# Kernel optimization log

Measured on AMD Instinct MI355X. Metric: run time of the kernel, lower is better.

The kernel has to match this reference:

```python
import jax, jax.numpy as jnp
import numpy as np

PAD = 2  # matches init_kwargs padding

# HEALPix face layout (DLWP-HEALPix / earth2grid convention):
#   faces 0-3 : northern polar cap
#   faces 4-7 : equatorial belt
#   faces 8-11: southern polar cap
# Padding each face gathers edge strips from topological neighbor faces;
# polar-cap neighbors require 90/180-degree rotations, and the two degenerate
# equatorial corners (touching a pole vertex, 3 faces meet) are filled with
# edge continuations + an averaged corner pixel.

def _rot(x, k):
    return jnp.rot90(x, k, axes=(-2, -1))

def _corner_tl(t, l, p):
    # degenerate top-left corner of an equatorial face (pole vertex)
    shp = t.shape[:-2] + (p, p)
    c = jnp.zeros(shp, t.dtype)
    c = c.at[..., :, -1].set(t[..., -p:, 0])          # continue top neighbor's left edge
    c = c.at[..., -1, :].set(l[..., 0, -p:])          # continue left neighbor's top edge
    c = c.at[..., -1, -1].set(0.5 * t[..., -1, 0] + 0.5 * l[..., 0, -1])
    return c

def _corner_br(b, r, p):
    # degenerate bottom-right corner of an equatorial face (pole vertex)
    shp = b.shape[:-2] + (p, p)
    c = jnp.zeros(shp, b.dtype)
    c = c.at[..., :, 0].set(b[..., :p, -1])
    c = c.at[..., 0, :].set(r[..., -1, :p])
    c = c.at[..., 0, 0].set(0.5 * b[..., 0, -1] + 0.5 * r[..., -1, 0])
    return c

def _assemble(tl, t, tr, l, c, r, bl, b, br):
    top = jnp.concatenate([tl, t, tr], axis=-1)
    mid = jnp.concatenate([l, c, r], axis=-1)
    bot = jnp.concatenate([bl, b, br], axis=-1)
    return jnp.concatenate([top, mid, bot], axis=-2)

def _pn(c, t, tl, l, bl, b, br, r, tr, p):
    # northern polar face: top/left neighbors are rotated polar faces
    return _assemble(
        _rot(tl, 2)[..., -p:, -p:], _rot(t, 1)[..., -p:, :], _rot(tr, 1)[..., -p:, :p],
        _rot(l, -1)[..., :, -p:],   c,                       r[..., :, :p],
        bl[..., :p, -p:],           b[..., :p, :],           br[..., :p, :p])

def _pe(c, t, tl, l, bl, b, br, r, tr, p):
    # equatorial face: no rotations; tl/br are precomputed degenerate corners
    return _assemble(
        tl,               t[..., -p:, :], tr[..., -p:, :p],
        l[..., :, -p:],   c,              r[..., :, :p],
        bl[..., :p, -p:], b[..., :p, :],  br)

def _ps(c, t, tl, l, bl, b, br, r, tr, p):
    # southern polar face: mirror image of the northern case
    return _assemble(
        tl[..., -p:, :p], t[..., -p:, :],        tr[..., -p:, -p:],
        l[..., :, -p:],   c,                     _rot(r, -1)[..., :, :p],
        _rot(bl, 1)[..., :p, -p:], _rot(b, 1)[..., :p, :], _rot(br, 2)[..., :p, :p])

def healpix_pad(x, p):
    # x: (B, 12, C, H, W) -> (B, 12, C, H+2p, W+2p)
    f = [x[:, i] for i in range(12)]
    out = []
    for i in range(4):  # northern cap faces 0..3
        out.append(_pn(f[i], t=f[(i + 1) % 4], tl=f[(i + 2) % 4], l=f[(i - 1) % 4],
                       bl=f[(i - 1) % 4], b=f[4 + i], br=f[8 + i],
                       r=f[4 + (i + 1) % 4], tr=f[(i + 1) % 4], p=p))
    for i in range(4):  # equatorial faces 4..7
        out.append(_pe(f[4 + i], t=f[i], tl=_corner_tl(f[i], f[(i - 1) % 4], p),
                       l=f[(i - 1) % 4], bl=f[4 + (i - 1) % 4], b=f[8 + i],
                       br=_corner_br(f[8 + i], f[8 + (i - 1) % 4], p),
                       r=f[4 + (i + 1) % 4], tr=f[i], p=p))
    for i in range(4):  # southern cap faces 8..11
        out.append(_ps(f[8 + i], t=f[4 + i], tl=f[4 + i], l=f[4 + (i + 1) % 4],
                       bl=f[8 + (i + 1) % 4], b=f[8 + (i - 1) % 4], br=f[8 + (i - 1) % 4],
                       r=f[8 + (i + 1) % 4], tr=f[i], p=p))
    return jnp.stack(out, axis=1)


def setup_inputs() -> dict:
    key = jax.random.key(0)
    x = jax.random.normal(key, (2, 12, 32, 256, 256), dtype=jnp.float32)
    return {"x": x}


def reference(x) -> jnp.ndarray:
    return healpix_pad(x, PAD)
```

## Files before the change

kernel.cpp:

```cpp
#include <hip/hip_runtime.h>


constexpr int N  = 256;
constexpr int P  = 2;
constexpr int NP = N + 2 * P;
constexpr int C  = 32;
constexpr int PLANE_OUT = NP * NP;
constexpr int PLANE_IN  = N * N;
constexpr int BULK_X    = 8;
constexpr int ITERS     = (N * (N / 4)) / (BULK_X * 256);

typedef float f32x4 __attribute__((ext_vector_type(4)));

__device__ __forceinline__ float gather(const float* __restrict__ in,
                                        int basePlane, int face, int i,
                                        int oh, int ow) {
    auto L = [&](int f, int sh, int sw) -> float {
        return in[(size_t)(basePlane + f * C) * PLANE_IN + sh * N + sw];
    };

    float v;
    if (face < 4) {
        if (oh < P) {
            if (ow < P)              v = L((i + 2) & 3, P - 1 - oh, P - 1 - ow);
            else if (ow < P + N)     v = L((i + 1) & 3, ow - P, P - 1 - oh);
            else                     v = L((i + 1) & 3, ow - P - N, P - 1 - oh);
        } else if (oh < P + N) {
            int ch = oh - P;
            if (ow < P)              v = L((i + 3) & 3, P - 1 - ow, ch);
            else if (ow < P + N)     v = L(face, ch, ow - P);
            else                     v = L(4 + ((i + 1) & 3), ch, ow - P - N);
        } else {
            int bh = oh - P - N;
            if (ow < P)              v = L((i + 3) & 3, bh, N - P + ow);
            else if (ow < P + N)     v = L(4 + i, bh, ow - P);
            else                     v = L(8 + i, bh, ow - P - N);
        }
    } else if (face < 8) {
        if (oh < P) {
            if (ow < P) {
                if (oh == P - 1 && ow == P - 1)
                    v = 0.5f * L(i, N - 1, 0) + 0.5f * L((i + 3) & 3, 0, N - 1);
                else if (oh == P - 1) v = L((i + 3) & 3, 0, N - P + ow);
                else if (ow == P - 1) v = L(i, N - P + oh, 0);
                else                  v = 0.0f;
            }
            else if (ow < P + N)     v = L(i, N - P + oh, ow - P);
            else                     v = L(i, N - P + oh, ow - P - N);
        } else if (oh < P + N) {
            int ch = oh - P;
            if (ow < P)              v = L((i + 3) & 3, ch, N - P + ow);
            else if (ow < P + N)     v = L(face, ch, ow - P);
            else                     v = L(4 + ((i + 1) & 3), ch, ow - P - N);
        } else {
            int bh = oh - P - N;
            if (ow < P)              v = L(4 + ((i + 3) & 3), bh, N - P + ow);
            else if (ow < P + N)     v = L(8 + i, bh, ow - P);
            else {
                int bw = ow - P - N;
                if (bh == 0 && bw == 0)
                    v = 0.5f * L(8 + i, 0, N - 1) + 0.5f * L(8 + ((i + 3) & 3), N - 1, 0);
                else if (bh == 0)     v = L(8 + ((i + 3) & 3), N - 1, bw);
                else if (bw == 0)     v = L(8 + i, bh, N - 1);
                else                  v = 0.0f;
            }
        }
    } else {
        if (oh < P) {
            if (ow < P)              v = L(4 + i, N - P + oh, ow);
            else if (ow < P + N)     v = L(4 + i, N - P + oh, ow - P);
            else                     v = L(i, N - P + oh, N - P + (ow - P - N));
        } else if (oh < P + N) {
            int ch = oh - P;
            if (ow < P)              v = L(4 + ((i + 1) & 3), ch, N - P + ow);
            else if (ow < P + N)     v = L(face, ch, ow - P);
            else {
                int bw = ow - P - N;
                v = L(8 + ((i + 1) & 3), N - 1 - bw, ch);
            }
        } else {
            int bh = oh - P - N;
            if (ow < P)              v = L(8 + ((i + 1) & 3), N - P + ow, N - 1 - bh);
            else if (ow < P + N)     v = L(8 + ((i + 3) & 3), ow - P, N - 1 - bh);
            else {
                int bw = ow - P - N;
                v = L(8 + ((i + 3) & 3), N - 1 - bh, N - 1 - bw);
            }
        }
    }
    return v;
}

__global__ __launch_bounds__(256)
void healpix_pad_kernel(const float* __restrict__ in, float* __restrict__ out) {
    const int plane = blockIdx.y;
    const int x     = blockIdx.x;

    float* __restrict__ oplane = out + (size_t)plane * PLANE_OUT;

    if (x < BULK_X) {
        const float* __restrict__ iplane = in + (size_t)plane * PLANE_IN;
        const int base = x * 256 + threadIdx.x;

        f32x4 v[ITERS];
        #pragma unroll
        for (int it = 0; it < ITERS; ++it) {
            int f4 = base + it * 2048;
            v[it] = *reinterpret_cast<const f32x4*>(iplane + f4 * 4);
        }
        #pragma unroll
        for (int it = 0; it < ITERS; ++it) {
            int f4  = base + it * 2048;
            int row = f4 >> 6;
            int c4  = f4 & 63;
            float* dst = oplane + (row + P) * NP + c4 * 4 + P;
            __builtin_nontemporal_store(v[it], reinterpret_cast<f32x4*>(dst));
        }
        return;
    }

    const int bc   = plane >> 5;
    const int face = bc >= 12 ? bc - 12 : bc;
    const int i    = face & 3;
    const int basePlane = plane - face * C;

    for (int t = threadIdx.x; t < 772; t += 256) {
        if (t < 260) {
            int row = (t < 130) ? (t / 65) : (258 + (t - 130) / 65);
            int j   = (t < 130) ? (t % 65) : ((t - 130) % 65);
            int ow  = 4 * j;
            f32x4 v;
            v.x = gather(in, basePlane, face, i, row, ow);
            v.y = gather(in, basePlane, face, i, row, ow + 1);
            v.z = gather(in, basePlane, face, i, row, ow + 2);
            v.w = gather(in, basePlane, face, i, row, ow + 3);
            *reinterpret_cast<f32x4*>(oplane + row * NP + ow) = v;
        } else if (t < 516) {
            int oh = (t - 260) + P;
            float2 v;
            v.x = gather(in, basePlane, face, i, oh, 0);
            v.y = gather(in, basePlane, face, i, oh, 1);
            *reinterpret_cast<float2*>(oplane + oh * NP) = v;
        } else {
            int oh = (t - 516) + P;
            float2 v;
            v.x = gather(in, basePlane, face, i, oh, NP - 2);
            v.y = gather(in, basePlane, face, i, oh, NP - 1);
            *reinterpret_cast<float2*>(oplane + oh * NP + NP - 2) = v;
        }
    }
}

extern "C" void kernel_launch(void* const* d_in, const int* in_sizes, int n_in,
                              void* d_out, int out_size, void* d_ws, size_t ws_size,
                              hipStream_t stream) {
    const float* in = (const float*)d_in[0];
    float* out = (float*)d_out;
    int planes = out_size / PLANE_OUT;
    dim3 block(256);
    dim3 grid(BULK_X + 1, planes);
    healpix_pad_kernel<<<grid, block, 0, stream>>>(in, out);
}
```

Measured before the change: 79.22 us.

## Write interior rows as full aligned output rows with fused side halos

The bulk path now gives each wavefront whole output rows. Each lane stores a 16-byte-aligned f32x4 to the padded output, built from two float2 input loads offset by the padding. Lane 0 also gathers the left and right halo columns, so the edge block only handles the top and bottom halo rows. This removes the earlier misaligned f32x4 stores (the output row pitch is 260 floats) and the separate column-halo passes, at the cost of more blocks per plane and unaligned half-width loads.

```diff
diff --git a/kernel.cpp b/kernel.cpp
--- a/kernel.cpp
+++ b/kernel.cpp
@@ -7,8 +7,7 @@
 constexpr int C  = 32;
 constexpr int PLANE_OUT = NP * NP;
 constexpr int PLANE_IN  = N * N;
-constexpr int BULK_X    = 8;
-constexpr int ITERS     = (N * (N / 4)) / (BULK_X * 256);
+constexpr int BULK_X    = 32;
 
 typedef float f32x4 __attribute__((ext_vector_type(4)));
 
@@ -97,57 +96,59 @@
     const int x     = blockIdx.x;
 
     float* __restrict__ oplane = out + (size_t)plane * PLANE_OUT;
-
-    if (x < BULK_X) {
-        const float* __restrict__ iplane = in + (size_t)plane * PLANE_IN;
-        const int base = x * 256 + threadIdx.x;
-
-        f32x4 v[ITERS];
-        #pragma unroll
-        for (int it = 0; it < ITERS; ++it) {
-            int f4 = base + it * 2048;
-            v[it] = *reinterpret_cast<const f32x4*>(iplane + f4 * 4);
-        }
-        #pragma unroll
-        for (int it = 0; it < ITERS; ++it) {
-            int f4  = base + it * 2048;
-            int row = f4 >> 6;
-            int c4  = f4 & 63;
-            float* dst = oplane + (row + P) * NP + c4 * 4 + P;
-            __builtin_nontemporal_store(v[it], reinterpret_cast<f32x4*>(dst));
-        }
-        return;
-    }
+    const float* __restrict__ iplane = in + (size_t)plane * PLANE_IN;
 
     const int bc   = plane >> 5;
     const int face = bc >= 12 ? bc - 12 : bc;
     const int i    = face & 3;
     const int basePlane = plane - face * C;
 
-    for (int t = threadIdx.x; t < 772; t += 256) {
-        if (t < 260) {
-            int row = (t < 130) ? (t / 65) : (258 + (t - 130) / 65);
-            int j   = (t < 130) ? (t % 65) : ((t - 130) % 65);
-            int ow  = 4 * j;
-            f32x4 v;
-            v.x = gather(in, basePlane, face, i, row, ow);
-            v.y = gather(in, basePlane, face, i, row, ow + 1);
-            v.z = gather(in, basePlane, face, i, row, ow + 2);
-            v.w = gather(in, basePlane, face, i, row, ow + 3);
-            *reinterpret_cast<f32x4*>(oplane + row * NP + ow) = v;
-        } else if (t < 516) {
-            int oh = (t - 260) + P;
-            float2 v;
-            v.x = gather(in, basePlane, face, i, oh, 0);
-            v.y = gather(in, basePlane, face, i, oh, 1);
-            *reinterpret_cast<float2*>(oplane + oh * NP) = v;
-        } else {
-            int oh = (t - 516) + P;
-            float2 v;
-            v.x = gather(in, basePlane, face, i, oh, NP - 2);
-            v.y = gather(in, basePlane, face, i, oh, NP - 1);
-            *reinterpret_cast<float2*>(oplane + oh * NP + NP - 2) = v;
+    if (x < BULK_X) {
+        const int w = threadIdx.x >> 6;
+        const int l = threadIdx.x & 63;
+        const int r0 = x * 8 + w;
+
+        #pragma unroll
+        for (int k = 0; k < 2; ++k) {
+            const int r  = r0 + 4 * k;
+            const int oh = r + P;
+            const float* __restrict__ src = iplane + r * N;
+            float* __restrict__ dst = oplane + oh * NP;
+
+            if (l != 0) {
+                float2 a = *reinterpret_cast<const float2*>(src + 4 * l - 2);
+                float2 b = *reinterpret_cast<const float2*>(src + 4 * l);
+                f32x4 v = {a.x, a.y, b.x, b.y};
+                __builtin_nontemporal_store(v, reinterpret_cast<f32x4*>(dst + 4 * l));
+            } else {
+                f32x4 v0;
+                v0.x = gather(in, basePlane, face, i, oh, 0);
+                v0.y = gather(in, basePlane, face, i, oh, 1);
+                float2 a = *reinterpret_cast<const float2*>(src);
+                v0.z = a.x; v0.w = a.y;
+                __builtin_nontemporal_store(v0, reinterpret_cast<f32x4*>(dst));
+                f32x4 v1;
+                float2 b = *reinterpret_cast<const float2*>(src + N - 2);
+                v1.x = b.x; v1.y = b.y;
+                v1.z = gather(in, basePlane, face, i, oh, NP - 2);
+                v1.w = gather(in, basePlane, face, i, oh, NP - 1);
+                __builtin_nontemporal_store(v1, reinterpret_cast<f32x4*>(dst + N));
+            }
         }
+        return;
+    }
+
+    for (int t = threadIdx.x; t < 4 * 65; t += 256) {
+        int q   = t / 65;
+        int row = (q < 2) ? q : 256 + q;
+        int j   = t - q * 65;
+        int ow  = 4 * j;
+        f32x4 v;
+        v.x = gather(in, basePlane, face, i, row, ow);
+        v.y = gather(in, basePlane, face, i, row, ow + 1);
+        v.z = gather(in, basePlane, face, i, row, ow + 2);
+        v.w = gather(in, basePlane, face, i, row, ow + 3);
+        __builtin_nontemporal_store(v, reinterpret_cast<f32x4*>(oplane + row * NP + ow));
     }
 }
 
```

Result: faster. 76.56 us (-3.4%).
